# Kernel optimization log

Measured on AMD Instinct MI355X. Metric: run time of the kernel, lower is better.

The kernel has to match this reference:

```python
import jax, jax.numpy as jnp
import numpy as np

N, E, F, H, C, G = 50000, 800000, 128, 1, 64, 256
NEG_SLOPE = 0.2


def _seg_softmax(e, seg, n):
    # numerically-stable softmax over edges grouped by target node
    m = jax.ops.segment_max(e, seg, num_segments=n)
    ex = jnp.exp(e - m[seg])
    s = jax.ops.segment_sum(ex, seg, num_segments=n)
    return ex / (s[seg] + 1e-16)


def _gatv2(x, src, dst, wl, bl, wr, br, att, bo, n):
    # GATv2Conv (PyG semantics): lin_l on source x_j, lin_r on target x_i
    xl = (x @ wl.T + bl).reshape(n, H, C)
    xr = (x @ wr.T + br).reshape(n, H, C)
    s = xl[src] + xr[dst]                      # [E, H, C]
    e = jnp.sum(jax.nn.leaky_relu(s, NEG_SLOPE) * att, axis=-1)  # [E, H]
    alpha = _seg_softmax(e, dst, n)
    out = jax.ops.segment_sum(alpha[..., None] * xl[src], dst, num_segments=n)
    return out.reshape(n, H * C) + bo


def setup_inputs() -> dict:
    key = jax.random.key(0)
    ks = jax.random.split(key, 24)
    d = {}
    d['x'] = jax.random.normal(ks[0], (N, F), dtype=jnp.float32)
    d['edge_index'] = jax.random.randint(ks[1], (2, E), 0, N)
    d['batch_idx'] = jnp.sort(jax.random.randint(ks[2], (N,), 0, G))
    sc = 0.1
    # conv1: in=F, out=C
    d['wl1'] = jax.random.normal(ks[3], (H * C, F)) * sc
    d['bl1'] = jnp.zeros((H * C,), jnp.float32)
    d['wr1'] = jax.random.normal(ks[4], (H * C, F)) * sc
    d['br1'] = jnp.zeros((H * C,), jnp.float32)
    d['att1'] = jax.random.normal(ks[5], (H, C)) * sc
    d['bo1'] = jnp.zeros((H * C,), jnp.float32)
    # conv2, conv3: in=H*C, out=C
    d['wl2'] = jax.random.normal(ks[6], (H * C, H * C)) * sc
    d['bl2'] = jnp.zeros((H * C,), jnp.float32)
    d['wr2'] = jax.random.normal(ks[7], (H * C, H * C)) * sc
    d['br2'] = jnp.zeros((H * C,), jnp.float32)
    d['att2'] = jax.random.normal(ks[8], (H, C)) * sc
    d['bo2'] = jnp.zeros((H * C,), jnp.float32)
    d['wl3'] = jax.random.normal(ks[9], (H * C, H * C)) * sc
    d['bl3'] = jnp.zeros((H * C,), jnp.float32)
    d['wr3'] = jax.random.normal(ks[10], (H * C, H * C)) * sc
    d['br3'] = jnp.zeros((H * C,), jnp.float32)
    d['att3'] = jax.random.normal(ks[11], (H, C)) * sc
    d['bo3'] = jnp.zeros((H * C,), jnp.float32)
    # heads
    d['lin1_w'] = jax.random.normal(ks[12], (C, 3 * H * C)) * sc
    d['lin1_b'] = jnp.zeros((C,), jnp.float32)
    d['pred_w'] = jax.random.normal(ks[13], (C, C)) * sc
    d['pred_b'] = jnp.zeros((C,), jnp.float32)
    d['cls_w'] = jax.random.normal(ks[14], (2, C)) * sc
    d['cls_b'] = jnp.zeros((2,), jnp.float32)
    return d


def reference(x, edge_index, batch_idx, wl1, bl1, wr1, br1, att1, bo1,
              wl2, bl2, wr2, br2, att2, bo2, wl3, bl3, wr3, br3, att3, bo3,
              lin1_w, lin1_b, pred_w, pred_b, cls_w, cls_b):
    # add self-loops (GATv2Conv default add_self_loops=True)
    loop = jnp.arange(N, dtype=edge_index.dtype)
    src = jnp.concatenate([edge_index[0], loop])
    dst = jnp.concatenate([edge_index[1], loop])
    x1 = jax.nn.relu(_gatv2(x, src, dst, wl1, bl1, wr1, br1, att1, bo1, N))
    x2 = jax.nn.relu(_gatv2(x1, src, dst, wl2, bl2, wr2, br2, att2, bo2, N))
    x3 = jax.nn.relu(_gatv2(x2, src, dst, wl3, bl3, wr3, br3, att3, bo3, N))
    h = jax.nn.relu(jnp.concatenate([x1, x2, x3], axis=1) @ lin1_w.T + lin1_b)
    g = jax.ops.segment_sum(h, batch_idx, num_segments=G)  # global_add_pool
    emb = jax.nn.relu(g @ pred_w.T + pred_b)                # pred_layer
    out = emb @ cls_w.T + cls_b                             # cls_layer
    return out
```

## Files before the change

kernel.cpp:

```cpp
#include <hip/hip_runtime.h>
#include <hip/hip_bf16.h>

#define N_NODES 50000
#define N_EDGES 800000
#define FDIM 128
#define CDIM 64
#define NGRAPH 256
#define LRELU_SLOPE 0.2f
#define NBUCK ((N_NODES + 255) / 256)
#define BCAP 5120
#define ABLK 400
#define EPB ((N_EDGES + ABLK - 1) / ABLK)
#define NDBIN 64
#define GEMMB ((N_NODES + 63) / 64)

typedef unsigned short ushort_t;
typedef unsigned int uint_t;
typedef __attribute__((ext_vector_type(8))) short short8v;
typedef __attribute__((ext_vector_type(4))) float float4v;

__device__ __forceinline__ ushort_t f2bf(float f) {
    uint_t u = __float_as_uint(f);
    u += 0x7FFFu + ((u >> 16) & 1u);
    return (ushort_t)(u >> 16);
}
__device__ __forceinline__ float bf2f(ushort_t u) {
    return __uint_as_float(((uint_t)u) << 16);
}

__device__ __forceinline__ float fast_exp2(float x) {
    return __builtin_amdgcn_exp2f(x);
}

__device__ __forceinline__ int wave_incl_scan(int v, int lane) {
#pragma unroll
    for (int off = 1; off < 64; off <<= 1) {
        int t = __shfl_up(v, off);
        if (lane >= off) v += t;
    }
    return v;
}

__device__ __forceinline__ float wave_sum(float v) {
#pragma unroll
    for (int off = 32; off >= 1; off >>= 1) v += __shfl_xor(v, off);
    return v;
}

__global__ void k_cvt_x(const float* __restrict__ x, ushort_t* __restrict__ xb) {
    int i = blockIdx.x * 256 + threadIdx.x;
    const int TOT = N_NODES * FDIM / 8;
    if (i >= TOT) return;
    const float* p = x + (size_t)i * 8;
    float4 a = *reinterpret_cast<const float4*>(p);
    float4 b = *reinterpret_cast<const float4*>(p + 4);
    short8v o;
    o[0] = (short)f2bf(a.x); o[1] = (short)f2bf(a.y);
    o[2] = (short)f2bf(a.z); o[3] = (short)f2bf(a.w);
    o[4] = (short)f2bf(b.x); o[5] = (short)f2bf(b.y);
    o[6] = (short)f2bf(b.z); o[7] = (short)f2bf(b.w);
    *reinterpret_cast<short8v*>(xb + (size_t)i * 8) = o;
}

__global__ void k_bucket(const int* __restrict__ src, const int* __restrict__ dst,
                         int* __restrict__ bcnt, int2* __restrict__ stage) {
    __shared__ int lhist[NBUCK];
    __shared__ int lbase[NBUCK];
    __shared__ int lcur[NBUCK];
    int tid = threadIdx.x;
    int e0 = blockIdx.x * EPB;
    int e1 = min(e0 + EPB, N_EDGES);
    for (int t = tid; t < NBUCK; t += 256) { lhist[t] = 0; lcur[t] = 0; }
    __syncthreads();
    for (int e = e0 + tid; e < e1; e += 256)
        atomicAdd(&lhist[dst[e] >> 8], 1);
    __syncthreads();
    for (int t = tid; t < NBUCK; t += 256)
        lbase[t] = atomicAdd(&bcnt[t], lhist[t]);
    __syncthreads();
    for (int e = e0 + tid; e < e1; e += 256) {
        int s = src[e], d = dst[e];
        int b = d >> 8;
        int loff = atomicAdd(&lcur[b], 1);
        int pos = lbase[b] + loff;
        if (pos < BCAP) stage[(size_t)b * BCAP + pos] = make_int2(s, d);
    }
}

__global__ void k_bscan(const int* __restrict__ bcnt, int* __restrict__ bbase) {
    __shared__ int wsum[4];
    int tid = threadIdx.x;
    int lane = tid & 63, w = tid >> 6;
    int v = (tid < NBUCK) ? bcnt[tid] : 0;
    int incl = wave_incl_scan(v, lane);
    if (lane == 63) wsum[w] = incl;
    __syncthreads();
    if (tid == 0) {
        int s = 0;
#pragma unroll
        for (int k = 0; k < 4; k++) { int t = wsum[k]; wsum[k] = s; s += t; }
    }
    __syncthreads();
    if (tid < NBUCK) bbase[tid] = incl - v + wsum[w];
}

__global__ void k_csr(const int* __restrict__ bcnt, const int* __restrict__ bbase,
                      const int2* __restrict__ stage, int* __restrict__ rowptr,
                      int* __restrict__ cnt, int* __restrict__ dhist,
                      int* __restrict__ csr_src) {
    __shared__ int lcnt[256];
    __shared__ int lcur[256];
    __shared__ int ldh[NDBIN];
    __shared__ int wsum[4];
    int b = blockIdx.x;
    int tid = threadIdx.x;
    int lane = tid & 63, w = tid >> 6;
    lcnt[tid] = 0;
    if (tid < NDBIN) ldh[tid] = 0;
    __syncthreads();
    int n = min(bcnt[b], BCAP);
    const int2* sp = stage + (size_t)b * BCAP;
    for (int i = tid; i < n; i += 256)
        atomicAdd(&lcnt[sp[i].y & 255], 1);
    __syncthreads();
    int v = lcnt[tid];
    int incl = wave_incl_scan(v, lane);
    if (lane == 63) wsum[w] = incl;
    __syncthreads();
    if (tid == 0) {
        int s = 0;
#pragma unroll
        for (int k = 0; k < 4; k++) { int t = wsum[k]; wsum[k] = s; s += t; }
    }
    __syncthreads();
    int excl = incl - v + wsum[w];
    int bb = bbase[b];
    int node = (b << 8) + tid;
    if (node < N_NODES) {
        rowptr[node] = bb + excl;
        cnt[node] = v;
        atomicAdd(&ldh[min(v, NDBIN - 1)], 1);
    }
    lcur[tid] = excl;
    __syncthreads();
    if (tid < NDBIN && ldh[tid]) atomicAdd(&dhist[tid], ldh[tid]);
    if (b == 0 && tid == 0) rowptr[N_NODES] = N_EDGES;
    for (int i = tid; i < n; i += 256) {
        int2 sd = sp[i];
        int pos = atomicAdd(&lcur[sd.y & 255], 1);
        csr_src[bb + pos] = sd.x;
    }
}

__global__ void k_scan2d(const int* __restrict__ dhist, int* __restrict__ dcur) {
    int lane = threadIdx.x;
    int v = dhist[lane];
    int incl = wave_incl_scan(v, lane);
    dcur[lane] = incl - v;
}

__global__ void k_dscatter(const int* __restrict__ cnt, int* __restrict__ dcur,
                           int* __restrict__ order) {
    __shared__ int lh[NDBIN], lb[NDBIN], lc[NDBIN];
    int b = blockIdx.x, tid = threadIdx.x;
    if (tid < NDBIN) { lh[tid] = 0; lc[tid] = 0; }
    __syncthreads();
    int node = b * 256 + tid;
    bool ok = node < N_NODES;
    int dg = ok ? min(cnt[node], NDBIN - 1) : 0;
    if (ok) atomicAdd(&lh[dg], 1);
    __syncthreads();
    if (tid < NDBIN) lb[tid] = lh[tid] ? atomicAdd(&dcur[tid], lh[tid]) : 0;
    __syncthreads();
    if (ok) {
        int off2 = atomicAdd(&lc[dg], 1);
        order[lb[dg] + off2] = node;
    }
}

struct WSrc {
    const float* s[7];
    int off[8];
};
__global__ void k_cvt_w(WSrc ws, ushort_t* __restrict__ hi, ushort_t* __restrict__ lo) {
    int gid = blockIdx.x * 256 + threadIdx.x;
    int stride = gridDim.x * 256;
#pragma unroll
    for (int mi = 0; mi < 7; mi++) {
        int n = ws.off[mi + 1] - ws.off[mi];
        const float* s = ws.s[mi];
        ushort_t* h = hi + ws.off[mi];
        ushort_t* l = lo + ws.off[mi];
        for (int i = gid; i < n; i += stride) {
            float f = s[i];
            ushort_t hb = f2bf(f);
            h[i] = hb;
            l[i] = f2bf(f - bf2f(hb));
        }
    }
}

template <int K>
__global__ void k_gemm_dual_mfma(const ushort_t* __restrict__ xa,
                                 const ushort_t* __restrict__ wlh, const ushort_t* __restrict__ wll,
                                 const ushort_t* __restrict__ wrh, const ushort_t* __restrict__ wrl,
                                 const float* __restrict__ bl, const float* __restrict__ br,
                                 ushort_t* __restrict__ xl, ushort_t* __restrict__ xr) {
    int tid = threadIdx.x;
    int wv = tid >> 6, lane = tid & 63;
    bool rhalf = blockIdx.x >= GEMMB;
    int blk = rhalf ? blockIdx.x - GEMMB : blockIdx.x;
    int m0 = blk * 64 + wv * 16;
    if (m0 >= N_NODES) return;
    int arow = min(m0 + (lane & 15), N_NODES - 1);
    int koff = (lane >> 4) * 8;
    int wrow = lane & 15;
    const ushort_t* bh  = rhalf ? wrh : wlh;
    const ushort_t* blo = rhalf ? wrl : wll;
    const float* bias   = rhalf ? br : bl;
    ushort_t* outp      = rhalf ? xr : xl;

    short8v afrag[K / 32];
#pragma unroll
    for (int kk = 0; kk < K / 32; kk++)
        afrag[kk] = *reinterpret_cast<const short8v*>(xa + (size_t)arow * K + kk * 32 + koff);

    float4v acc[4];
#pragma unroll
    for (int f = 0; f < 4; f++) acc[f] = (float4v)(0.f);

#pragma unroll
    for (int kk = 0; kk < K / 32; kk++) {
#pragma unroll
        for (int f = 0; f < 4; f++) {
            size_t boff = (size_t)(f * 16 + wrow) * K + kk * 32 + koff;
            short8v bfh = *reinterpret_cast<const short8v*>(bh + boff);
            short8v bfl = *reinterpret_cast<const short8v*>(blo + boff);
            acc[f] = __builtin_amdgcn_mfma_f32_16x16x32_bf16(afrag[kk], bfh, acc[f], 0, 0, 0);
            acc[f] = __builtin_amdgcn_mfma_f32_16x16x32_bf16(afrag[kk], bfl, acc[f], 0, 0, 0);
        }
    }

    int r0 = m0 + (lane >> 4) * 4;
#pragma unroll
    for (int f = 0; f < 4; f++) {
        int col = f * 16 + (lane & 15);
        float bv = bias[col];
#pragma unroll
        for (int j = 0; j < 4; j++) {
            int row = r0 + j;
            if (row < N_NODES) outp[(size_t)row * 64 + col] = f2bf(acc[f][j] + bv);
        }
    }
}

__global__ void k_gemm_h_pool(const ushort_t* __restrict__ x1, const ushort_t* __restrict__ x2,
                              const ushort_t* __restrict__ x3,
                              const ushort_t* __restrict__ whi, const ushort_t* __restrict__ wlo,
                              const float* __restrict__ b, const int* __restrict__ batch,
                              float* __restrict__ g) {
    __shared__ float ht[64][65];
    int tid = threadIdx.x;
    int wv = tid >> 6, lane = tid & 63;
    int m0 = blockIdx.x * 64 + wv * 16;
    bool wactive = m0 < N_NODES;

    if (wactive) {
        int arow = min(m0 + (lane & 15), N_NODES - 1);
        int koff = (lane >> 4) * 8;
        int wrow = lane & 15;
        float4v acc[4];
#pragma unroll
        for (int f = 0; f < 4; f++) acc[f] = (float4v)(0.f);
#pragma unroll
        for (int ks = 0; ks < 6; ks++) {
            int k0 = ks * 32;
            const ushort_t* srcp = (ks < 2) ? x1 : (ks < 4 ? x2 : x3);
            int kc = k0 & 63;
            short8v afrag = *reinterpret_cast<const short8v*>(srcp + (size_t)arow * 64 + kc + koff);
#pragma unroll
            for (int f = 0; f < 4; f++) {
                size_t boff = (size_t)(f * 16 + wrow) * 192 + k0 + koff;
                short8v bfh = *reinterpret_cast<const short8v*>(whi + boff);
                short8v bfl = *reinterpret_cast<const short8v*>(wlo + boff);
                acc[f] = __builtin_amdgcn_mfma_f32_16x16x32_bf16(afrag, bfh, acc[f], 0, 0, 0);
                acc[f] = __builtin_amdgcn_mfma_f32_16x16x32_bf16(afrag, bfl, acc[f], 0, 0, 0);
            }
        }
        int r0 = wv * 16 + (lane >> 4) * 4;
#pragma unroll
        for (int f = 0; f < 4; f++) {
            int col = f * 16 + (lane & 15);
            float bias = b[col];
#pragma unroll
            for (int j = 0; j < 4; j++) {
                float o = acc[f][j] + bias;
                ht[r0 + j][col] = o > 0.f ? o : 0.f;
            }
        }
    }
    __syncthreads();

    int c = tid & 63, rr = tid >> 6;
    int blkbase = blockIdx.x * 64;
    float acc = 0.f;
    int cur = -1;
    for (int r = rr; r < 64; r += 4) {
        int node = blkbase + r;
        if (node >= N_NODES) break;
        int bb = batch[node];
        if (bb != cur) {
            if (cur >= 0) atomicAdd(&g[cur * 64 + c], acc);
            cur = bb;
            acc = 0.f;
        }
        acc += ht[r][c];
    }
    if (cur >= 0) atomicAdd(&g[cur * 64 + c], acc);
}

__global__ void k_gat(const ushort_t* __restrict__ xl, const ushort_t* __restrict__ xr,
                      const int* __restrict__ rowptr, const int* __restrict__ csr_src,
                      const int* __restrict__ order,
                      const float* __restrict__ att, const float* __restrict__ bo,
                      ushort_t* __restrict__ xout) {
    int tid = threadIdx.x;
    int wv = tid >> 6, lane = tid & 63;
    int gl = lane & 15;
    int slot = blockIdx.x * 16 + wv * 4 + (lane >> 4);
    if (slot >= N_NODES) return;
    int node = order[slot];
    const float LOG2E = 1.44269504f;
    int c0 = gl * 4;
    float4 a4 = *reinterpret_cast<const float4*>(att + c0);
    float at0 = a4.x * LOG2E, at1 = a4.y * LOG2E, at2 = a4.z * LOG2E, at3 = a4.w * LOG2E;
    size_t nb = (size_t)node * 64 + c0;
    ushort4 qr = *reinterpret_cast<const ushort4*>(xr + nb);
    ushort4 ql = *reinterpret_cast<const ushort4*>(xl + nb);
    float xr0 = bf2f(qr.x), xr1 = bf2f(qr.y), xr2 = bf2f(qr.z), xr3 = bf2f(qr.w);
    float l0 = bf2f(ql.x), l1 = bf2f(ql.y), l2 = bf2f(ql.z), l3 = bf2f(ql.w);

    auto grd = [](float p) {
        p += __shfl_xor(p, 1);
        p += __shfl_xor(p, 2);
        p += __shfl_xor(p, 4);
        p += __shfl_xor(p, 8);
        return p;
    };
    auto score4 = [&](float v0, float v1, float v2, float v3) {
        float s0 = v0 + xr0, s1 = v1 + xr1, s2 = v2 + xr2, s3 = v3 + xr3;
        float t0 = fmaxf(s0, LRELU_SLOPE * s0);
        float t1 = fmaxf(s1, LRELU_SLOPE * s1);
        float t2 = fmaxf(s2, LRELU_SLOPE * s2);
        float t3 = fmaxf(s3, LRELU_SLOPE * s3);
        return ((t0 * at0 + t1 * at1) + (t2 * at2 + t3 * at3));
    };

    int beg = rowptr[node], end = rowptr[node + 1];
    int deg = end - beg;
    int lim = end - 1;

    float m = grd(score4(l0, l1, l2, l3));
    float ssum = 1.f;
    float a0 = l0, a1 = l1, a2 = l2, a3 = l3;

    for (int j = 0; j < deg; j += 8) {
        int base = beg + j;
        int i0 = base;
        int i1 = min(base + 1, lim), i2 = min(base + 2, lim), i3 = min(base + 3, lim);
        int i4 = min(base + 4, lim), i5 = min(base + 5, lim);
        int i6 = min(base + 6, lim), i7 = min(base + 7, lim);
        int s0 = csr_src[i0], s1 = csr_src[i1], s2 = csr_src[i2], s3 = csr_src[i3];
        int s4 = csr_src[i4], s5 = csr_src[i5], s6 = csr_src[i6], s7 = csr_src[i7];
        ushort4 q0 = *reinterpret_cast<const ushort4*>(xl + (size_t)s0 * 64 + c0);
        ushort4 q1 = *reinterpret_cast<const ushort4*>(xl + (size_t)s1 * 64 + c0);
        ushort4 q2 = *reinterpret_cast<const ushort4*>(xl + (size_t)s2 * 64 + c0);
        ushort4 q3 = *reinterpret_cast<const ushort4*>(xl + (size_t)s3 * 64 + c0);
        ushort4 q4 = *reinterpret_cast<const ushort4*>(xl + (size_t)s4 * 64 + c0);
        ushort4 q5 = *reinterpret_cast<const ushort4*>(xl + (size_t)s5 * 64 + c0);
        ushort4 q6 = *reinterpret_cast<const ushort4*>(xl + (size_t)s6 * 64 + c0);
        ushort4 q7 = *reinterpret_cast<const ushort4*>(xl + (size_t)s7 * 64 + c0);
        float v00 = bf2f(q0.x), v01 = bf2f(q0.y), v02 = bf2f(q0.z), v03 = bf2f(q0.w);
        float v10 = bf2f(q1.x), v11 = bf2f(q1.y), v12 = bf2f(q1.z), v13 = bf2f(q1.w);
        float v20 = bf2f(q2.x), v21 = bf2f(q2.y), v22 = bf2f(q2.z), v23 = bf2f(q2.w);
        float v30 = bf2f(q3.x), v31 = bf2f(q3.y), v32 = bf2f(q3.z), v33 = bf2f(q3.w);
        float v40 = bf2f(q4.x), v41 = bf2f(q4.y), v42 = bf2f(q4.z), v43 = bf2f(q4.w);
        float v50 = bf2f(q5.x), v51 = bf2f(q5.y), v52 = bf2f(q5.z), v53 = bf2f(q5.w);
        float v60 = bf2f(q6.x), v61 = bf2f(q6.y), v62 = bf2f(q6.z), v63 = bf2f(q6.w);
        float v70 = bf2f(q7.x), v71 = bf2f(q7.y), v72 = bf2f(q7.z), v73 = bf2f(q7.w);
        float e0 = grd(score4(v00, v01, v02, v03));
        float e1 = grd(score4(v10, v11, v12, v13));
        float e2 = grd(score4(v20, v21, v22, v23));
        float e3 = grd(score4(v30, v31, v32, v33));
        float e4 = grd(score4(v40, v41, v42, v43));
        float e5 = grd(score4(v50, v51, v52, v53));
        float e6 = grd(score4(v60, v61, v62, v63));
        float e7 = grd(score4(v70, v71, v72, v73));
        int rem = deg - j;
        if (rem < 8) {
            e1 = (rem > 1) ? e1 : -1e30f;
            e2 = (rem > 2) ? e2 : -1e30f;
            e3 = (rem > 3) ? e3 : -1e30f;
            e4 = (rem > 4) ? e4 : -1e30f;
            e5 = (rem > 5) ? e5 : -1e30f;
            e6 = (rem > 6) ? e6 : -1e30f;
            e7 = (rem > 7) ? e7 : -1e30f;
        }
        float mx = fmaxf(fmaxf(fmaxf(e0, e1), fmaxf(e2, e3)),
                         fmaxf(fmaxf(e4, e5), fmaxf(e6, e7)));
        float mn = fmaxf(m, mx);
        float sc = fast_exp2(m - mn);
        float w0 = fast_exp2(e0 - mn), w1 = fast_exp2(e1 - mn);
        float w2 = fast_exp2(e2 - mn), w3 = fast_exp2(e3 - mn);
        float w4 = fast_exp2(e4 - mn), w5 = fast_exp2(e5 - mn);
        float w6 = fast_exp2(e6 - mn), w7 = fast_exp2(e7 - mn);
        ssum = ssum * sc + (((w0 + w1) + (w2 + w3)) + ((w4 + w5) + (w6 + w7)));
        a0 = a0 * sc + (((w0 * v00 + w1 * v10) + (w2 * v20 + w3 * v30)) +
                        ((w4 * v40 + w5 * v50) + (w6 * v60 + w7 * v70)));
        a1 = a1 * sc + (((w0 * v01 + w1 * v11) + (w2 * v21 + w3 * v31)) +
                        ((w4 * v41 + w5 * v51) + (w6 * v61 + w7 * v71)));
        a2 = a2 * sc + (((w0 * v02 + w1 * v12) + (w2 * v22 + w3 * v32)) +
                        ((w4 * v42 + w5 * v52) + (w6 * v62 + w7 * v72)));
        a3 = a3 * sc + (((w0 * v03 + w1 * v13) + (w2 * v23 + w3 * v33)) +
                        ((w4 * v43 + w5 * v53) + (w6 * v63 + w7 * v73)));
        m = mn;
    }

    float rs = 1.f / (ssum + 1e-16f);
    float4 b4 = *reinterpret_cast<const float4*>(bo + c0);
    float o0 = fmaxf(a0 * rs + b4.x, 0.f);
    float o1 = fmaxf(a1 * rs + b4.y, 0.f);
    float o2 = fmaxf(a2 * rs + b4.z, 0.f);
    float o3 = fmaxf(a3 * rs + b4.w, 0.f);
    ushort4 oq;
    oq.x = f2bf(o0); oq.y = f2bf(o1); oq.z = f2bf(o2); oq.w = f2bf(o3);
    *reinterpret_cast<ushort4*>(xout + nb) = oq;
}

__global__ void k_head(const float* __restrict__ g, const float* __restrict__ pw,
                       const float* __restrict__ pb, const float* __restrict__ cw,
                       const float* __restrict__ cb, float* __restrict__ out) {
    int gb = blockIdx.x;
    int c = threadIdx.x;
    const float* gr = g + gb * 64;
    float a = pb[c];
    const float* pwr = pw + c * 64;
#pragma unroll
    for (int k = 0; k < 64; k++) a += gr[k] * pwr[k];
    a = a > 0.f ? a : 0.f;
    float o0 = wave_sum(a * cw[c]);
    float o1 = wave_sum(a * cw[64 + c]);
    if (c == 0) {
        out[gb * 2 + 0] = o0 + cb[0];
        out[gb * 2 + 1] = o1 + cb[1];
    }
}

extern "C" void kernel_launch(void* const* d_in, const int* in_sizes, int n_in,
                              void* d_out, int out_size, void* d_ws, size_t ws_size,
                              hipStream_t stream) {
    const float* x    = (const float*)d_in[0];
    const int*   ei   = (const int*)d_in[1];
    const int*   bidx = (const int*)d_in[2];
    const float* wl1 = (const float*)d_in[3],  *bl1 = (const float*)d_in[4];
    const float* wr1 = (const float*)d_in[5],  *br1 = (const float*)d_in[6];
    const float* att1 = (const float*)d_in[7], *bo1 = (const float*)d_in[8];
    const float* wl2 = (const float*)d_in[9],  *bl2 = (const float*)d_in[10];
    const float* wr2 = (const float*)d_in[11], *br2 = (const float*)d_in[12];
    const float* att2 = (const float*)d_in[13], *bo2 = (const float*)d_in[14];
    const float* wl3 = (const float*)d_in[15], *bl3 = (const float*)d_in[16];
    const float* wr3 = (const float*)d_in[17], *br3 = (const float*)d_in[18];
    const float* att3 = (const float*)d_in[19], *bo3 = (const float*)d_in[20];
    const float* lw = (const float*)d_in[21], *lb = (const float*)d_in[22];
    const float* pw = (const float*)d_in[23], *pb = (const float*)d_in[24];
    const float* cw = (const float*)d_in[25], *cb = (const float*)d_in[26];
    float* out = (float*)d_out;

    char* wsb = (char*)d_ws;
    size_t off = 0;
    auto alloc = [&](size_t bytes) {
        void* p = wsb + off;
        off = (off + bytes + 255) & ~(size_t)255;
        return p;
    };
    int* cnt      = (int*)alloc((size_t)N_NODES * 4);
    int* rowptr   = (int*)alloc((size_t)(N_NODES + 1) * 4);
    int* bcnt     = (int*)alloc((size_t)(NBUCK + NDBIN) * 4);
    int* dhist    = bcnt + NBUCK;
    int* bbase    = (int*)alloc((size_t)NBUCK * 4);
    int* dcur     = (int*)alloc((size_t)NDBIN * 4);
    int* order    = (int*)alloc((size_t)N_NODES * 4);
    int2* stage   = (int2*)alloc((size_t)NBUCK * BCAP * 8);
    int* csr_src  = (int*)alloc((size_t)N_EDGES * 4);
    const int woff[8] = {0, 8192, 16384, 20480, 24576, 28672, 32768, 45056};
    ushort_t* whi = (ushort_t*)alloc((size_t)45056 * 2);
    ushort_t* wlo = (ushort_t*)alloc((size_t)45056 * 2);
    ushort_t* xbf  = (ushort_t*)alloc((size_t)N_NODES * FDIM * 2);
    ushort_t* xl   = (ushort_t*)alloc((size_t)N_NODES * 64 * 2);
    ushort_t* xrr  = (ushort_t*)alloc((size_t)N_NODES * 64 * 2);
    ushort_t* x1b  = (ushort_t*)alloc((size_t)N_NODES * 64 * 2);
    ushort_t* x2b  = (ushort_t*)alloc((size_t)N_NODES * 64 * 2);
    ushort_t* x3b  = (ushort_t*)alloc((size_t)N_NODES * 64 * 2);
    float* g      = (float*)alloc((size_t)NGRAPH * 64 * 4);
    (void)ws_size; (void)in_sizes; (void)n_in; (void)out_size;

    const int* srcp = ei;
    const int* dstp = ei + N_EDGES;

    hipMemsetAsync(bcnt, 0, (size_t)(NBUCK + NDBIN) * 4, stream);
    hipMemsetAsync(g, 0, (size_t)NGRAPH * 64 * 4, stream);

    k_bucket<<<ABLK, 256, 0, stream>>>(srcp, dstp, bcnt, stage);
    k_bscan<<<1, 256, 0, stream>>>(bcnt, bbase);
    k_csr<<<NBUCK, 256, 0, stream>>>(bcnt, bbase, stage, rowptr, cnt, dhist, csr_src);
    k_scan2d<<<1, 64, 0, stream>>>(dhist, dcur);
    k_dscatter<<<NBUCK, 256, 0, stream>>>(cnt, dcur, order);

    WSrc ws;
    ws.s[0] = wl1; ws.s[1] = wr1; ws.s[2] = wl2; ws.s[3] = wr2;
    ws.s[4] = wl3; ws.s[5] = wr3; ws.s[6] = lw;
    for (int i = 0; i < 8; i++) ws.off[i] = woff[i];
    k_cvt_w<<<64, 256, 0, stream>>>(ws, whi, wlo);
    k_cvt_x<<<(N_NODES * FDIM / 8 + 255) / 256, 256, 0, stream>>>(x, xbf);

    int gatBlocks = (N_NODES + 15) / 16;

    k_gemm_dual_mfma<128><<<2 * GEMMB, 256, 0, stream>>>(
        xbf, whi + woff[0], wlo + woff[0], whi + woff[1], wlo + woff[1], bl1, br1, xl, xrr);
    k_gat<<<gatBlocks, 256, 0, stream>>>(xl, xrr, rowptr, csr_src, order, att1, bo1, x1b);
    k_gemm_dual_mfma<64><<<2 * GEMMB, 256, 0, stream>>>(
        x1b, whi + woff[2], wlo + woff[2], whi + woff[3], wlo + woff[3], bl2, br2, xl, xrr);
    k_gat<<<gatBlocks, 256, 0, stream>>>(xl, xrr, rowptr, csr_src, order, att2, bo2, x2b);
    k_gemm_dual_mfma<64><<<2 * GEMMB, 256, 0, stream>>>(
        x2b, whi + woff[4], wlo + woff[4], whi + woff[5], wlo + woff[5], bl3, br3, xl, xrr);
    k_gat<<<gatBlocks, 256, 0, stream>>>(xl, xrr, rowptr, csr_src, order, att3, bo3, x3b);

    k_gemm_h_pool<<<GEMMB, 256, 0, stream>>>(x1b, x2b, x3b, whi + woff[6], wlo + woff[6],
                                             lb, bidx, g);
    k_head<<<NGRAPH, 64, 0, stream>>>(g, pw, pb, cw, cb, out);
}
```

Measured before the change: 254.0 us.

## Prefetch CSR indices in GAT loop, localize degree sort, trim preprocessing launches

```diff
diff --git a/kernel.cpp b/kernel.cpp
--- a/kernel.cpp
+++ b/kernel.cpp
@@ -70,24 +70,35 @@
     int tid = threadIdx.x;
     int e0 = blockIdx.x * EPB;
     int e1 = min(e0 + EPB, N_EDGES);
+    int es[8], ed[8];
+    int myn = 0;
+#pragma unroll
+    for (int k = 0; k < 8; k++) {
+        int e = e0 + tid + k * 256;
+        if (e < e1) { es[k] = src[e]; ed[k] = dst[e]; myn = k + 1; }
+    }
     for (int t = tid; t < NBUCK; t += 256) { lhist[t] = 0; lcur[t] = 0; }
     __syncthreads();
-    for (int e = e0 + tid; e < e1; e += 256)
-        atomicAdd(&lhist[dst[e] >> 8], 1);
+#pragma unroll
+    for (int k = 0; k < 8; k++)
+        if (k < myn) atomicAdd(&lhist[ed[k] >> 8], 1);
     __syncthreads();
     for (int t = tid; t < NBUCK; t += 256)
-        lbase[t] = atomicAdd(&bcnt[t], lhist[t]);
-    __syncthreads();
-    for (int e = e0 + tid; e < e1; e += 256) {
-        int s = src[e], d = dst[e];
-        int b = d >> 8;
-        int loff = atomicAdd(&lcur[b], 1);
-        int pos = lbase[b] + loff;
-        if (pos < BCAP) stage[(size_t)b * BCAP + pos] = make_int2(s, d);
-    }
-}
-
-__global__ void k_bscan(const int* __restrict__ bcnt, int* __restrict__ bbase) {
+        lbase[t] = lhist[t] ? atomicAdd(&bcnt[t], lhist[t]) : 0;
+    __syncthreads();
+#pragma unroll
+    for (int k = 0; k < 8; k++) {
+        if (k < myn) {
+            int b = ed[k] >> 8;
+            int loff = atomicAdd(&lcur[b], 1);
+            int pos = lbase[b] + loff;
+            if (pos < BCAP) stage[(size_t)b * BCAP + pos] = make_int2(es[k], ed[k]);
+        }
+    }
+}
+
+__global__ void k_bscan(const int* __restrict__ bcnt, int* __restrict__ bbase,
+                        float4* __restrict__ g4) {
     __shared__ int wsum[4];
     int tid = threadIdx.x;
     int lane = tid & 63, w = tid >> 6;
@@ -102,21 +113,23 @@
     }
     __syncthreads();
     if (tid < NBUCK) bbase[tid] = incl - v + wsum[w];
+    const int G4 = NGRAPH * 64 / 4;
+    for (int i = tid; i < G4; i += 256) g4[i] = make_float4(0.f, 0.f, 0.f, 0.f);
 }
 
 __global__ void k_csr(const int* __restrict__ bcnt, const int* __restrict__ bbase,
                       const int2* __restrict__ stage, int* __restrict__ rowptr,
-                      int* __restrict__ cnt, int* __restrict__ dhist,
-                      int* __restrict__ csr_src) {
+                      int* __restrict__ order, int* __restrict__ csr_src) {
     __shared__ int lcnt[256];
     __shared__ int lcur[256];
-    __shared__ int ldh[NDBIN];
+    __shared__ int dh[NDBIN];
+    __shared__ int dbase[NDBIN];
     __shared__ int wsum[4];
     int b = blockIdx.x;
     int tid = threadIdx.x;
     int lane = tid & 63, w = tid >> 6;
     lcnt[tid] = 0;
-    if (tid < NDBIN) ldh[tid] = 0;
+    if (tid < NDBIN) dh[tid] = 0;
     __syncthreads();
     int n = min(bcnt[b], BCAP);
     const int2* sp = stage + (size_t)b * BCAP;
@@ -136,45 +149,29 @@
     int excl = incl - v + wsum[w];
     int bb = bbase[b];
     int node = (b << 8) + tid;
-    if (node < N_NODES) {
+    bool okn = node < N_NODES;
+    int dg = min(v, NDBIN - 1);
+    if (okn) {
         rowptr[node] = bb + excl;
-        cnt[node] = v;
-        atomicAdd(&ldh[min(v, NDBIN - 1)], 1);
+        atomicAdd(&dh[dg], 1);
     }
     lcur[tid] = excl;
-    __syncthreads();
-    if (tid < NDBIN && ldh[tid]) atomicAdd(&dhist[tid], ldh[tid]);
     if (b == 0 && tid == 0) rowptr[N_NODES] = N_EDGES;
+    __syncthreads();
+    if (tid < NDBIN) {
+        int dv = dh[tid];
+        int din = wave_incl_scan(dv, tid);
+        dbase[tid] = din - dv;
+    }
+    __syncthreads();
+    if (okn) {
+        int r = atomicAdd(&dbase[dg], 1);
+        order[(b << 8) + r] = node;
+    }
     for (int i = tid; i < n; i += 256) {
         int2 sd = sp[i];
         int pos = atomicAdd(&lcur[sd.y & 255], 1);
         csr_src[bb + pos] = sd.x;
-    }
-}
-
-__global__ void k_scan2d(const int* __restrict__ dhist, int* __restrict__ dcur) {
-    int lane = threadIdx.x;
-    int v = dhist[lane];
-    int incl = wave_incl_scan(v, lane);
-    dcur[lane] = incl - v;
-}
-
-__global__ void k_dscatter(const int* __restrict__ cnt, int* __restrict__ dcur,
-                           int* __restrict__ order) {
-    __shared__ int lh[NDBIN], lb[NDBIN], lc[NDBIN];
-    int b = blockIdx.x, tid = threadIdx.x;
-    if (tid < NDBIN) { lh[tid] = 0; lc[tid] = 0; }
-    __syncthreads();
-    int node = b * 256 + tid;
-    bool ok = node < N_NODES;
-    int dg = ok ? min(cnt[node], NDBIN - 1) : 0;
-    if (ok) atomicAdd(&lh[dg], 1);
-    __syncthreads();
-    if (tid < NDBIN) lb[tid] = lh[tid] ? atomicAdd(&dcur[tid], lh[tid]) : 0;
-    __syncthreads();
-    if (ok) {
-        int off2 = atomicAdd(&lc[dg], 1);
-        order[lb[dg] + off2] = node;
     }
 }
 
@@ -364,66 +361,86 @@
     float ssum = 1.f;
     float a0 = l0, a1 = l1, a2 = l2, a3 = l3;
 
-    for (int j = 0; j < deg; j += 8) {
-        int base = beg + j;
-        int i0 = base;
-        int i1 = min(base + 1, lim), i2 = min(base + 2, lim), i3 = min(base + 3, lim);
-        int i4 = min(base + 4, lim), i5 = min(base + 5, lim);
-        int i6 = min(base + 6, lim), i7 = min(base + 7, lim);
-        int s0 = csr_src[i0], s1 = csr_src[i1], s2 = csr_src[i2], s3 = csr_src[i3];
-        int s4 = csr_src[i4], s5 = csr_src[i5], s6 = csr_src[i6], s7 = csr_src[i7];
-        ushort4 q0 = *reinterpret_cast<const ushort4*>(xl + (size_t)s0 * 64 + c0);
-        ushort4 q1 = *reinterpret_cast<const ushort4*>(xl + (size_t)s1 * 64 + c0);
-        ushort4 q2 = *reinterpret_cast<const ushort4*>(xl + (size_t)s2 * 64 + c0);
-        ushort4 q3 = *reinterpret_cast<const ushort4*>(xl + (size_t)s3 * 64 + c0);
-        ushort4 q4 = *reinterpret_cast<const ushort4*>(xl + (size_t)s4 * 64 + c0);
-        ushort4 q5 = *reinterpret_cast<const ushort4*>(xl + (size_t)s5 * 64 + c0);
-        ushort4 q6 = *reinterpret_cast<const ushort4*>(xl + (size_t)s6 * 64 + c0);
-        ushort4 q7 = *reinterpret_cast<const ushort4*>(xl + (size_t)s7 * 64 + c0);
-        float v00 = bf2f(q0.x), v01 = bf2f(q0.y), v02 = bf2f(q0.z), v03 = bf2f(q0.w);
-        float v10 = bf2f(q1.x), v11 = bf2f(q1.y), v12 = bf2f(q1.z), v13 = bf2f(q1.w);
-        float v20 = bf2f(q2.x), v21 = bf2f(q2.y), v22 = bf2f(q2.z), v23 = bf2f(q2.w);
-        float v30 = bf2f(q3.x), v31 = bf2f(q3.y), v32 = bf2f(q3.z), v33 = bf2f(q3.w);
-        float v40 = bf2f(q4.x), v41 = bf2f(q4.y), v42 = bf2f(q4.z), v43 = bf2f(q4.w);
-        float v50 = bf2f(q5.x), v51 = bf2f(q5.y), v52 = bf2f(q5.z), v53 = bf2f(q5.w);
-        float v60 = bf2f(q6.x), v61 = bf2f(q6.y), v62 = bf2f(q6.z), v63 = bf2f(q6.w);
-        float v70 = bf2f(q7.x), v71 = bf2f(q7.y), v72 = bf2f(q7.z), v73 = bf2f(q7.w);
-        float e0 = grd(score4(v00, v01, v02, v03));
-        float e1 = grd(score4(v10, v11, v12, v13));
-        float e2 = grd(score4(v20, v21, v22, v23));
-        float e3 = grd(score4(v30, v31, v32, v33));
-        float e4 = grd(score4(v40, v41, v42, v43));
-        float e5 = grd(score4(v50, v51, v52, v53));
-        float e6 = grd(score4(v60, v61, v62, v63));
-        float e7 = grd(score4(v70, v71, v72, v73));
-        int rem = deg - j;
-        if (rem < 8) {
-            e1 = (rem > 1) ? e1 : -1e30f;
-            e2 = (rem > 2) ? e2 : -1e30f;
-            e3 = (rem > 3) ? e3 : -1e30f;
-            e4 = (rem > 4) ? e4 : -1e30f;
-            e5 = (rem > 5) ? e5 : -1e30f;
-            e6 = (rem > 6) ? e6 : -1e30f;
-            e7 = (rem > 7) ? e7 : -1e30f;
-        }
-        float mx = fmaxf(fmaxf(fmaxf(e0, e1), fmaxf(e2, e3)),
-                         fmaxf(fmaxf(e4, e5), fmaxf(e6, e7)));
-        float mn = fmaxf(m, mx);
-        float sc = fast_exp2(m - mn);
-        float w0 = fast_exp2(e0 - mn), w1 = fast_exp2(e1 - mn);
-        float w2 = fast_exp2(e2 - mn), w3 = fast_exp2(e3 - mn);
-        float w4 = fast_exp2(e4 - mn), w5 = fast_exp2(e5 - mn);
-        float w6 = fast_exp2(e6 - mn), w7 = fast_exp2(e7 - mn);
-        ssum = ssum * sc + (((w0 + w1) + (w2 + w3)) + ((w4 + w5) + (w6 + w7)));
-        a0 = a0 * sc + (((w0 * v00 + w1 * v10) + (w2 * v20 + w3 * v30)) +
-                        ((w4 * v40 + w5 * v50) + (w6 * v60 + w7 * v70)));
-        a1 = a1 * sc + (((w0 * v01 + w1 * v11) + (w2 * v21 + w3 * v31)) +
-                        ((w4 * v41 + w5 * v51) + (w6 * v61 + w7 * v71)));
-        a2 = a2 * sc + (((w0 * v02 + w1 * v12) + (w2 * v22 + w3 * v32)) +
-                        ((w4 * v42 + w5 * v52) + (w6 * v62 + w7 * v72)));
-        a3 = a3 * sc + (((w0 * v03 + w1 * v13) + (w2 * v23 + w3 * v33)) +
-                        ((w4 * v43 + w5 * v53) + (w6 * v63 + w7 * v73)));
-        m = mn;
+    if (deg > 0) {
+        int sidx[16];
+#pragma unroll
+        for (int k = 0; k < 16; k++) sidx[k] = csr_src[min(beg + k, lim)];
+
+        for (int j = 0; j < deg; j += 16) {
+            ushort4 q[16];
+#pragma unroll
+            for (int k = 0; k < 16; k++)
+                q[k] = *reinterpret_cast<const ushort4*>(xl + (size_t)sidx[k] * 64 + c0);
+            int nidx[16];
+#pragma unroll
+            for (int k = 0; k < 16; k++) nidx[k] = csr_src[min(beg + j + 16 + k, lim)];
+
+            int rem = deg - j;
+
+            {
+                float vv[8][4], e_[8];
+#pragma unroll
+                for (int k = 0; k < 8; k++) {
+                    vv[k][0] = bf2f(q[k].x); vv[k][1] = bf2f(q[k].y);
+                    vv[k][2] = bf2f(q[k].z); vv[k][3] = bf2f(q[k].w);
+                    e_[k] = grd(score4(vv[k][0], vv[k][1], vv[k][2], vv[k][3]));
+                }
+#pragma unroll
+                for (int k = 1; k < 8; k++) if (k >= rem) e_[k] = -1e30f;
+                float mx = fmaxf(fmaxf(fmaxf(e_[0], e_[1]), fmaxf(e_[2], e_[3])),
+                                 fmaxf(fmaxf(e_[4], e_[5]), fmaxf(e_[6], e_[7])));
+                float mn = fmaxf(m, mx);
+                float sc = fast_exp2(m - mn);
+                float wgt[8];
+#pragma unroll
+                for (int k = 0; k < 8; k++) wgt[k] = fast_exp2(e_[k] - mn);
+                float sw = ((wgt[0] + wgt[1]) + (wgt[2] + wgt[3])) +
+                           ((wgt[4] + wgt[5]) + (wgt[6] + wgt[7]));
+                ssum = ssum * sc + sw;
+                a0 = a0 * sc + (((wgt[0] * vv[0][0] + wgt[1] * vv[1][0]) + (wgt[2] * vv[2][0] + wgt[3] * vv[3][0])) +
+                                ((wgt[4] * vv[4][0] + wgt[5] * vv[5][0]) + (wgt[6] * vv[6][0] + wgt[7] * vv[7][0])));
+                a1 = a1 * sc + (((wgt[0] * vv[0][1] + wgt[1] * vv[1][1]) + (wgt[2] * vv[2][1] + wgt[3] * vv[3][1])) +
+                                ((wgt[4] * vv[4][1] + wgt[5] * vv[5][1]) + (wgt[6] * vv[6][1] + wgt[7] * vv[7][1])));
+                a2 = a2 * sc + (((wgt[0] * vv[0][2] + wgt[1] * vv[1][2]) + (wgt[2] * vv[2][2] + wgt[3] * vv[3][2])) +
+                                ((wgt[4] * vv[4][2] + wgt[5] * vv[5][2]) + (wgt[6] * vv[6][2] + wgt[7] * vv[7][2])));
+                a3 = a3 * sc + (((wgt[0] * vv[0][3] + wgt[1] * vv[1][3]) + (wgt[2] * vv[2][3] + wgt[3] * vv[3][3])) +
+                                ((wgt[4] * vv[4][3] + wgt[5] * vv[5][3]) + (wgt[6] * vv[6][3] + wgt[7] * vv[7][3])));
+                m = mn;
+            }
+            if (rem > 8) {
+                float vv[8][4], e_[8];
+#pragma unroll
+                for (int k = 0; k < 8; k++) {
+                    vv[k][0] = bf2f(q[8 + k].x); vv[k][1] = bf2f(q[8 + k].y);
+                    vv[k][2] = bf2f(q[8 + k].z); vv[k][3] = bf2f(q[8 + k].w);
+                    e_[k] = grd(score4(vv[k][0], vv[k][1], vv[k][2], vv[k][3]));
+                }
+#pragma unroll
+                for (int k = 1; k < 8; k++) if (8 + k >= rem) e_[k] = -1e30f;
+                float mx = fmaxf(fmaxf(fmaxf(e_[0], e_[1]), fmaxf(e_[2], e_[3])),
+                                 fmaxf(fmaxf(e_[4], e_[5]), fmaxf(e_[6], e_[7])));
+                float mn = fmaxf(m, mx);
+                float sc = fast_exp2(m - mn);
+                float wgt[8];
+#pragma unroll
+                for (int k = 0; k < 8; k++) wgt[k] = fast_exp2(e_[k] - mn);
+                float sw = ((wgt[0] + wgt[1]) + (wgt[2] + wgt[3])) +
+                           ((wgt[4] + wgt[5]) + (wgt[6] + wgt[7]));
+                ssum = ssum * sc + sw;
+                a0 = a0 * sc + (((wgt[0] * vv[0][0] + wgt[1] * vv[1][0]) + (wgt[2] * vv[2][0] + wgt[3] * vv[3][0])) +
+                                ((wgt[4] * vv[4][0] + wgt[5] * vv[5][0]) + (wgt[6] * vv[6][0] + wgt[7] * vv[7][0])));
+                a1 = a1 * sc + (((wgt[0] * vv[0][1] + wgt[1] * vv[1][1]) + (wgt[2] * vv[2][1] + wgt[3] * vv[3][1])) +
+                                ((wgt[4] * vv[4][1] + wgt[5] * vv[5][1]) + (wgt[6] * vv[6][1] + wgt[7] * vv[7][1])));
+                a2 = a2 * sc + (((wgt[0] * vv[0][2] + wgt[1] * vv[1][2]) + (wgt[2] * vv[2][2] + wgt[3] * vv[3][2])) +
+                                ((wgt[4] * vv[4][2] + wgt[5] * vv[5][2]) + (wgt[6] * vv[6][2] + wgt[7] * vv[7][2])));
+                a3 = a3 * sc + (((wgt[0] * vv[0][3] + wgt[1] * vv[1][3]) + (wgt[2] * vv[2][3] + wgt[3] * vv[3][3])) +
+                                ((wgt[4] * vv[4][3] + wgt[5] * vv[5][3]) + (wgt[6] * vv[6][3] + wgt[7] * vv[7][3])));
+                m = mn;
+            }
+
+#pragma unroll
+            for (int k = 0; k < 16; k++) sidx[k] = nidx[k];
+        }
     }
 
     float rs = 1.f / (ssum + 1e-16f);
@@ -483,12 +500,9 @@
         off = (off + bytes + 255) & ~(size_t)255;
         return p;
     };
-    int* cnt      = (int*)alloc((size_t)N_NODES * 4);
     int* rowptr   = (int*)alloc((size_t)(N_NODES + 1) * 4);
-    int* bcnt     = (int*)alloc((size_t)(NBUCK + NDBIN) * 4);
-    int* dhist    = bcnt + NBUCK;
+    int* bcnt     = (int*)alloc((size_t)NBUCK * 4);
     int* bbase    = (int*)alloc((size_t)NBUCK * 4);
-    int* dcur     = (int*)alloc((size_t)NDBIN * 4);
     int* order    = (int*)alloc((size_t)N_NODES * 4);
     int2* stage   = (int2*)alloc((size_t)NBUCK * BCAP * 8);
     int* csr_src  = (int*)alloc((size_t)N_EDGES * 4);
@@ -507,14 +521,11 @@
     const int* srcp = ei;
     const int* dstp = ei + N_EDGES;
 
-    hipMemsetAsync(bcnt, 0, (size_t)(NBUCK + NDBIN) * 4, stream);
-    hipMemsetAsync(g, 0, (size_t)NGRAPH * 64 * 4, stream);
+    hipMemsetAsync(bcnt, 0, (size_t)NBUCK * 4, stream);
 
     k_bucket<<<ABLK, 256, 0, stream>>>(srcp, dstp, bcnt, stage);
-    k_bscan<<<1, 256, 0, stream>>>(bcnt, bbase);
-    k_csr<<<NBUCK, 256, 0, stream>>>(bcnt, bbase, stage, rowptr, cnt, dhist, csr_src);
-    k_scan2d<<<1, 64, 0, stream>>>(dhist, dcur);
-    k_dscatter<<<NBUCK, 256, 0, stream>>>(cnt, dcur, order);
+    k_bscan<<<1, 256, 0, stream>>>(bcnt, bbase, (float4*)g);
+    k_csr<<<NBUCK, 256, 0, stream>>>(bcnt, bbase, stage, rowptr, order, csr_src);
 
     WSrc ws;
     ws.s[0] = wl1; ws.s[1] = wr1; ws.s[2] = wl2; ws.s[3] = wr2;
```

Result: slower. 259.2 us (+2.0%).
